# Performance work log

Measured on AMD Instinct MI355X. Metric: run time of the kernel, lower is better.

## Reference

```python
import jax, jax.numpy as jnp
import numpy as np

DIM = 2048
H = 16
QLR = 1536
KVLR = 512
NOPE = 128
ROPE = 64
VH = 128
QKH = NOPE + ROPE  # 192
B, S = 2, 2048
EPS = 1e-6


def _rmsnorm(x, w):
    return x * jax.lax.rsqrt(jnp.mean(x * x, axis=-1, keepdims=True) + EPS) * w


def _rope_cos_sin(seq_len, r, dtype):
    inv_freq = 1.0 / (10000.0 ** (jnp.arange(0, r, 2, dtype=jnp.float32) / r))
    ang = jnp.arange(seq_len, dtype=jnp.float32)[:, None] * inv_freq  # [S, r/2]
    return jnp.cos(ang).astype(dtype), jnp.sin(ang).astype(dtype)


def _rot(t, cos, sin):
    # rotate-half RoPE on last dim; cos/sin pre-broadcast to t's rank
    t1, t2 = jnp.split(t, 2, axis=-1)
    return jnp.concatenate([t1 * cos - t2 * sin, t2 * cos + t1 * sin], axis=-1)


def setup_inputs() -> dict:
    key = jax.random.key(0)
    ks = jax.random.split(key, 12)
    sd = 0.02
    return {
        "x": jax.random.normal(ks[0], (B, S, DIM), jnp.float32),
        "wqd": jax.random.normal(ks[1], (DIM, QLR), jnp.float32) * sd,
        "bqd": jnp.zeros((QLR,), jnp.float32),
        "qnorm_w": jnp.ones((QLR,), jnp.float32),
        "wqu": jax.random.normal(ks[2], (QLR, H * QKH), jnp.float32) * sd,
        "bqu": jnp.zeros((H * QKH,), jnp.float32),
        "wkvd": jax.random.normal(ks[3], (DIM, KVLR + ROPE), jnp.float32) * sd,
        "bkvd": jnp.zeros((KVLR + ROPE,), jnp.float32),
        "kvnorm_w": jnp.ones((KVLR,), jnp.float32),
        "wkvu": jax.random.normal(ks[4], (KVLR, H * (NOPE + VH)), jnp.float32) * sd,
        "bkvu": jnp.zeros((H * (NOPE + VH),), jnp.float32),
        "wout": jax.random.normal(ks[5], (H * VH, DIM), jnp.float32) * sd,
        "bout": jnp.zeros((DIM,), jnp.float32),
    }


def reference(x, wqd, bqd, qnorm_w, wqu, bqu, wkvd, bkvd, kvnorm_w, wkvu, bkvu, wout, bout):
    b, s, _ = x.shape
    # Q path: low-rank down, RMSNorm, up; split nope / rope
    q = _rmsnorm(x @ wqd + bqd, qnorm_w) @ wqu + bqu        # [b,s,H*QKH]
    q = q.reshape(b, s, H, QKH)
    q_nope, q_rope = q[..., :NOPE], q[..., NOPE:]
    # KV path: joint down-proj -> kv latent + shared rope key
    kvd = x @ wkvd + bkvd                                   # [b,s,KVLR+ROPE]
    kv_lora, k_rope = kvd[..., :KVLR], kvd[..., KVLR:]
    cos, sin = _rope_cos_sin(s, ROPE, x.dtype)
    q_rope = _rot(q_rope, cos[None, :, None, :], sin[None, :, None, :])
    k_rope = _rot(k_rope, cos[None, :, :], sin[None, :, :])  # [b,s,ROPE]
    kvu = _rmsnorm(kv_lora, kvnorm_w) @ wkvu + bkvu          # [b,s,H*(NOPE+VH)]
    kvu = kvu.reshape(b, s, H, NOPE + VH)
    k_nope, v = kvu[..., :NOPE], kvu[..., NOPE:]
    k_rope_b = jnp.broadcast_to(k_rope[:, :, None, :], (b, s, H, ROPE))
    qf = jnp.concatenate([q_nope, q_rope], axis=-1)          # [b,s,H,QKH]
    kf = jnp.concatenate([k_nope, k_rope_b], axis=-1)        # [b,s,H,QKH]
    scale = QKH ** -0.5
    scores = jnp.einsum('bqhd,bkhd->bhqk', qf, kf) * scale
    causal = jnp.tril(jnp.ones((s, s), bool))
    scores = jnp.where(causal, scores, jnp.finfo(scores.dtype).min)
    attn = jax.nn.softmax(scores, axis=-1)
    o = jnp.einsum('bhqk,bkhd->bqhd', attn, v).reshape(b, s, H * VH)
    return o @ wout + bout
```

## Files before the change

### kernel.cpp

```cpp
#include <hip/hip_runtime.h>
#include <hip/hip_bf16.h>
#include <math.h>

#define HH 16
#define SS 2048
#define BBATCH 2
#define NROWS 4096

typedef __attribute__((ext_vector_type(8))) __bf16 bf16x8;
typedef __attribute__((ext_vector_type(4))) float f32x4;
typedef const __attribute__((address_space(1))) unsigned int* gas1_t;
typedef __attribute__((address_space(3))) unsigned int* las3_t;

__device__ __forceinline__ unsigned short f2bf(float f) {
  unsigned u = __builtin_bit_cast(unsigned, f);
  u += 0x7fffu + ((u >> 16) & 1u);
  return (unsigned short)(u >> 16);
}

__device__ __forceinline__ void gload16(const void* g, void* l) {
  __builtin_amdgcn_global_load_lds((gas1_t)g, (las3_t)l, 16, 0, 0);
}
__device__ __forceinline__ f32x4 mfma16(bf16x8 a, bf16x8 b, f32x4 c) {
  return __builtin_amdgcn_mfma_f32_16x16x32_bf16(a, b, c, 0, 0, 0);
}

__global__ __launch_bounds__(256) void k_convert(const float* __restrict__ in,
                                                 unsigned short* __restrict__ out, long n4) {
  long i = (long)blockIdx.x * blockDim.x + threadIdx.x;
  long stride = (long)gridDim.x * blockDim.x;
  for (; i < n4; i += stride) {
    float4 v = ((const float4*)in)[i];
    ushort4 o = { f2bf(v.x), f2bf(v.y), f2bf(v.z), f2bf(v.w) };
    ((ushort4*)out)[i] = o;
  }
}

__global__ __launch_bounds__(256) void k_transpose(const float* __restrict__ W,
                                                   unsigned short* __restrict__ Wt,
                                                   int K, int N, int Npad) {
  __shared__ float tile[32][33];
  int n0 = blockIdx.x * 32, k0 = blockIdx.y * 32;
  int tx = threadIdx.x & 31, ty = threadIdx.x >> 5;
  for (int i = ty; i < 32; i += 8) {
    int k = k0 + i, n = n0 + tx;
    tile[i][tx] = (k < K && n < N) ? W[(long)k * N + n] : 0.f;
  }
  __syncthreads();
  for (int i = ty; i < 32; i += 8) {
    int n = n0 + i, k = k0 + tx;
    if (n < Npad && k < K) Wt[(long)n * K + k] = f2bf(tile[tx][i]);
  }
}

__global__ __launch_bounds__(256) void k_bias_merge(const float* __restrict__ bqd,
                                                    const float* __restrict__ bkvd,
                                                    float* __restrict__ mb) {
  int i = blockIdx.x * 256 + threadIdx.x;
  if (i < 2176) mb[i] = i < 1536 ? bqd[i] : (i < 2112 ? bkvd[i - 1536] : 0.f);
}

__global__ __launch_bounds__(64) void k_rope_table(float2* __restrict__ tab) {
  int s = blockIdx.x * 2 + (threadIdx.x >> 5);
  int i = threadIdx.x & 31;
  float inv = powf(10000.f, -(float)i / 32.f);
  float ang = (float)s * inv;
  float sn, cs;
  sincosf(ang, &sn, &cs);
  tab[s * 32 + i] = make_float2(cs, sn);
}

__global__ __launch_bounds__(256) void k_gemm(const unsigned short* __restrict__ A,
                                              const unsigned short* __restrict__ Bt,
                                              const float* __restrict__ bias,
                                              float* __restrict__ C,
                                              int M, int N, int K) {
  __shared__ unsigned short lA[128 * 32];
  __shared__ unsigned short lB[128 * 32];
  int tid = threadIdx.x;
  int wave = tid >> 6, lane = tid & 63;
  int l15 = lane & 15, lhi = lane >> 4;
  int ntn = (N + 127) >> 7;
  int tm = blockIdx.x / ntn, tn = blockIdx.x % ntn;
  long row0 = (long)tm * 128, col0 = (long)tn * 128;
  int wr = wave >> 1, wc = wave & 1;

  const unsigned short* gA = A + (row0 + (tid >> 2)) * K + (tid & 3) * 8;
  const unsigned short* gB = Bt + (col0 + (tid >> 2)) * K + (tid & 3) * 8;
  unsigned short* lA0 = &lA[tid * 8];
  unsigned short* lB0 = &lB[tid * 8];

  f32x4 acc[4][4] = {};
  for (int k0 = 0; k0 < K; k0 += 32) {
    __syncthreads();
    gload16(gA + k0, lA0);
    gload16(gA + (long)64 * K + k0, lA0 + 2048);
    gload16(gB + k0, lB0);
    gload16(gB + (long)64 * K + k0, lB0 + 2048);
    asm volatile("s_waitcnt vmcnt(0)" ::: "memory");
    __syncthreads();
    bf16x8 af[4], bfr[4];
#pragma unroll
    for (int i = 0; i < 4; ++i) {
      af[i]  = *(const bf16x8*)&lA[(wr * 64 + i * 16 + l15) * 32 + lhi * 8];
      bfr[i] = *(const bf16x8*)&lB[(wc * 64 + i * 16 + l15) * 32 + lhi * 8];
    }
#pragma unroll
    for (int i = 0; i < 4; ++i)
#pragma unroll
      for (int j = 0; j < 4; ++j)
        acc[i][j] = mfma16(af[i], bfr[j], acc[i][j]);
  }
#pragma unroll
  for (int i = 0; i < 4; ++i)
#pragma unroll
    for (int j = 0; j < 4; ++j) {
      long r = row0 + wr * 64 + i * 16 + lhi * 4;
      long c = col0 + wc * 64 + j * 16 + l15;
      if (c < N) {
        float bv = bias[c];
#pragma unroll
        for (int rr = 0; rr < 4; ++rr)
          C[(r + rr) * N + c] = acc[i][j][rr] + bv;
      }
    }
}

__global__ __launch_bounds__(256) void k_gemm_qf(const unsigned short* __restrict__ A,
                                                 const unsigned short* __restrict__ Bt,
                                                 const float* __restrict__ bias,
                                                 const float2* __restrict__ rtab,
                                                 unsigned short* __restrict__ qf,
                                                 int M, int N, int K) {
  __shared__ unsigned short lA[128 * 32];
  __shared__ unsigned short lB[128 * 32];
  int tid = threadIdx.x;
  int wave = tid >> 6, lane = tid & 63;
  int l15 = lane & 15, lhi = lane >> 4;
  int ntn = (N + 127) >> 7;
  int tm = blockIdx.x / ntn, tn = blockIdx.x % ntn;
  long row0 = (long)tm * 128, col0 = (long)tn * 128;
  int wr = wave >> 1, wc = wave & 1;

  const unsigned short* gA = A + (row0 + (tid >> 2)) * K + (tid & 3) * 8;
  const unsigned short* gB = Bt + (col0 + (tid >> 2)) * K + (tid & 3) * 8;
  unsigned short* lA0 = &lA[tid * 8];
  unsigned short* lB0 = &lB[tid * 8];

  f32x4 acc[4][4] = {};
  for (int k0 = 0; k0 < K; k0 += 32) {
    __syncthreads();
    gload16(gA + k0, lA0);
    gload16(gA + (long)64 * K + k0, lA0 + 2048);
    gload16(gB + k0, lB0);
    gload16(gB + (long)64 * K + k0, lB0 + 2048);
    asm volatile("s_waitcnt vmcnt(0)" ::: "memory");
    __syncthreads();
    bf16x8 af[4], bfr[4];
#pragma unroll
    for (int i = 0; i < 4; ++i) {
      af[i]  = *(const bf16x8*)&lA[(wr * 64 + i * 16 + l15) * 32 + lhi * 8];
      bfr[i] = *(const bf16x8*)&lB[(wc * 64 + i * 16 + l15) * 32 + lhi * 8];
    }
#pragma unroll
    for (int i = 0; i < 4; ++i)
#pragma unroll
      for (int j = 0; j < 4; ++j)
        acc[i][j] = mfma16(af[i], bfr[j], acc[i][j]);
  }

  const float scq = 0.07216878364870322f * 1.4426950408889634f;
  int base = (int)col0 + wc * 64;
  int h = base / 192;
  int m192 = base - h * 192;
  float bv[4];
#pragma unroll
  for (int j = 0; j < 4; ++j) bv[j] = bias[base + j * 16 + l15];

#pragma unroll
  for (int i = 0; i < 4; ++i) {
#pragma unroll
    for (int rr = 0; rr < 4; ++rr) {
      long r = row0 + wr * 64 + i * 16 + lhi * 4 + rr;
      int s = (int)(r & 2047), b = (int)(r >> 11);
      unsigned short* dst = qf + (((long)(b * HH + h)) * SS + s) * 192;
      if (m192 < 128) {
#pragma unroll
        for (int j = 0; j < 4; ++j)
          dst[m192 + j * 16 + l15] = f2bf((acc[i][j][rr] + bv[j]) * scq);
      } else {
#pragma unroll
        for (int j = 0; j < 2; ++j) {
          int ifq = j * 16 + l15;
          float2 cs = rtab[s * 32 + ifq];
          float v1 = acc[i][j][rr] + bv[j];
          float v2 = acc[i][j + 2][rr] + bv[j + 2];
          dst[128 + ifq] = f2bf((v1 * cs.x - v2 * cs.y) * scq);
          dst[160 + ifq] = f2bf((v2 * cs.x + v1 * cs.y) * scq);
        }
      }
    }
  }
}

__global__ __launch_bounds__(256) void k_gemm_kv(const unsigned short* __restrict__ A,
                                                 const unsigned short* __restrict__ Bt,
                                                 const float* __restrict__ bias,
                                                 unsigned short* __restrict__ kf3,
                                                 unsigned short* __restrict__ vt3,
                                                 int M, int N, int K) {
  __shared__ unsigned short smem[16384];
  unsigned short* lA = smem;
  unsigned short* lB = smem + 4096;
  int tid = threadIdx.x;
  int wave = tid >> 6, lane = tid & 63;
  int l15 = lane & 15, lhi = lane >> 4;
  int ntn = N >> 7;
  int tm = blockIdx.x / ntn, tn = blockIdx.x % ntn;
  long row0 = (long)tm * 128, col0 = (long)tn * 128;
  int wr = wave >> 1, wc = wave & 1;

  const unsigned short* gA = A + (row0 + (tid >> 2)) * K + (tid & 3) * 8;
  const unsigned short* gB = Bt + (col0 + (tid >> 2)) * K + (tid & 3) * 8;
  unsigned short* lA0 = &lA[tid * 8];
  unsigned short* lB0 = &lB[tid * 8];

  f32x4 acc[4][4] = {};
  for (int k0 = 0; k0 < K; k0 += 32) {
    __syncthreads();
    gload16(gA + k0, lA0);
    gload16(gA + (long)64 * K + k0, lA0 + 2048);
    gload16(gB + k0, lB0);
    gload16(gB + (long)64 * K + k0, lB0 + 2048);
    asm volatile("s_waitcnt vmcnt(0)" ::: "memory");
    __syncthreads();
    bf16x8 af[4], bfr[4];
#pragma unroll
    for (int i = 0; i < 4; ++i) {
      af[i]  = *(const bf16x8*)&lA[(wr * 64 + i * 16 + l15) * 32 + lhi * 8];
      bfr[i] = *(const bf16x8*)&lB[(wc * 64 + i * 16 + l15) * 32 + lhi * 8];
    }
#pragma unroll
    for (int i = 0; i < 4; ++i)
#pragma unroll
      for (int j = 0; j < 4; ++j)
        acc[i][j] = mfma16(af[i], bfr[j], acc[i][j]);
  }

  int base = (int)col0 + wc * 64;
  int h = base >> 8;
  bool isv = (base & 255) >= 128;
  float bv[4];
#pragma unroll
  for (int j = 0; j < 4; ++j) bv[j] = bias[base + j * 16 + l15];

  int b = (int)(row0 >> 11);
  long bh = (long)b * HH + h;
  int lrb = wr * 64;
  __syncthreads();

  if (isv) {
#pragma unroll
    for (int i = 0; i < 4; ++i) {
      int lr = lrb + i * 16 + lhi * 4;
#pragma unroll
      for (int j = 0; j < 4; ++j) {
        int lc = wc * 64 + j * 16 + l15;
        ushort4 pk = { f2bf(acc[i][j][0] + bv[j]), f2bf(acc[i][j][1] + bv[j]),
                       f2bf(acc[i][j][2] + bv[j]), f2bf(acc[i][j][3] + bv[j]) };
        *(ushort4*)&smem[((lr >> 5) << 12) + lc * 32 + (lr & 31)] = pk;
      }
    }
    __syncthreads();
    long dst0 = (bh * 64 + ((row0 & 2047) >> 5)) * 4096;
#pragma unroll
    for (int p = 0; p < 8; ++p) {
      int e = p * 256 + tid;
      *(uint4*)&vt3[dst0 + e * 8] = *(uint4*)&smem[e * 8];
    }
  } else {
#pragma unroll
    for (int i = 0; i < 4; ++i) {
      int lr0 = lrb + i * 16 + lhi * 4;
#pragma unroll
      for (int j = 0; j < 4; ++j) {
        int c = (base & 255) + j * 16 + l15;
        int tbase = ((lr0 >> 4) << 11) + ((c >> 5) << 9) + (((c >> 3) & 3) << 7) + (c & 7);
#pragma unroll
        for (int rr = 0; rr < 4; ++rr)
          smem[tbase + ((lr0 + rr) & 15) * 8] = f2bf(acc[i][j][rr] + bv[j]);
      }
    }
    __syncthreads();
    long kb3 = (bh * 128 + ((row0 & 2047) >> 4)) * 3072;
#pragma unroll
    for (int p = 0; p < 8; ++p) {
      int e = p * 256 + tid;
      int tile = e >> 6;
      int off = (e & 63) * 8;
      long dst = kb3 + ((long)(tile >> 2) * 6 + (tile & 3)) * 512 + off;
      *(uint4*)&kf3[dst] = *(uint4*)&smem[tile * 512 + off];
    }
  }
}

__global__ __launch_bounds__(256) void k_rmsnorm(const float* __restrict__ X,
                                                 const float* __restrict__ w,
                                                 unsigned short* __restrict__ Y,
                                                 int L, int ldx) {
  long row = blockIdx.x;
  const float* x = X + row * ldx;
  float ss = 0.f;
  int n4 = L >> 2;
  for (int i = threadIdx.x; i < n4; i += 256) {
    float4 v = ((const float4*)x)[i];
    ss += v.x * v.x + v.y * v.y + v.z * v.z + v.w * v.w;
  }
  for (int off = 32; off > 0; off >>= 1) ss += __shfl_xor(ss, off);
  __shared__ float sb[4];
  if ((threadIdx.x & 63) == 0) sb[threadIdx.x >> 6] = ss;
  __syncthreads();
  float scale = rsqrtf((sb[0] + sb[1] + sb[2] + sb[3]) / (float)L + 1e-6f);
  unsigned short* y = Y + row * L;
  for (int i = threadIdx.x; i < L; i += 256)
    y[i] = f2bf(x[i] * scale * w[i]);
}

__global__ __launch_bounds__(64) void k_extract_krope(const float* __restrict__ sC,
                                                      unsigned short* __restrict__ kf3) {
  int bs = blockIdx.x;
  int lane = threadIdx.x;
  int s = bs & (SS - 1), b = bs >> 11;
  const float* src = sC + (long)bs * 2176 + 2048;
  int i = lane & 31;
  float inv = powf(10000.f, -(float)i / 32.f);
  float ang = (float)s * inv;
  float sn, cs;
  sincosf(ang, &sn, &cs);
  float t1 = src[i], t2 = src[32 + i];
  float v = (lane < 32) ? (t1 * cs - t2 * sn) : (t2 * cs + t1 * sn);
  unsigned short bv = f2bf(v);
  int d = 128 + lane;
  long inner = (long)(d >> 5) * 512 + ((d >> 3) & 3) * 128 + (s & 15) * 8 + (d & 7);
#pragma unroll
  for (int h = 0; h < HH; ++h) {
    long blk = ((long)(b * HH + h) * 128 + (s >> 4)) * 6;
    kf3[blk * 512 + inner] = bv;
  }
}

__global__ __launch_bounds__(256, 4) void k_attn(const unsigned short* __restrict__ qf,
                                                 const unsigned short* __restrict__ kf3,
                                                 const unsigned short* __restrict__ vt3,
                                                 unsigned short* __restrict__ o) {
  __shared__ unsigned short kbuf[64 * 192];
  __shared__ unsigned short pbuf[4][16 * 72];
  int tid = threadIdx.x;
  int wave = tid >> 6, lane = tid & 63;
  int l15 = lane & 15, lhi = lane >> 4;
  int idx = blockIdx.x;
  int g = idx >> 8, j = idx & 255;
  int a = j >> 5, bh = j & 31;
  int qt = g < 2 ? (g == 0 ? a : a + 8) : (g == 2 ? 23 - a : 31 - a);
  int b = bh >> 4, h = bh & 15;
  int q0 = qt * 64;
  int nt = qt + 1;
  const char* kbase = (const char*)(kf3 + (long)bh * 128 * 3072);
  const unsigned short* vfrag0 = vt3 + (long)bh * 64 * 4096 + l15 * 32 + lhi * 8;
  const unsigned short* kread = kbuf + lane * 8;

  {
    const char* src = kbase + tid * 16;
    char* dst = (char*)kbuf + tid * 16;
#pragma unroll
    for (int p = 0; p < 6; ++p) gload16(src + p * 4096, dst + p * 4096);
  }

  const unsigned short* Qb = qf + ((long)bh * SS + q0 + wave * 16 + l15) * 192 + lhi * 8;
  bf16x8 qfr[6];
#pragma unroll
  for (int ks = 0; ks < 6; ++ks) qfr[ks] = *(const bf16x8*)(Qb + ks * 32);

  float m = -3e38f, ls = 0.f;
  f32x4 acc[8] = {};
  int qin = wave * 16 + l15;

  for (int t = 0; t < nt; ++t) {
    asm volatile("s_waitcnt vmcnt(0)" ::: "memory");
    __builtin_amdgcn_s_barrier();
    __builtin_amdgcn_sched_barrier(0);

    f32x4 sc[4] = {};
    __builtin_amdgcn_s_setprio(1);
#pragma unroll
    for (int ks = 0; ks < 6; ++ks) {
      bf16x8 kfr[4];
#pragma unroll
      for (int nf = 0; nf < 4; ++nf)
        kfr[nf] = *(const bf16x8*)&kread[(nf * 6 + ks) * 512];
#pragma unroll
      for (int nf = 0; nf < 4; ++nf)
        sc[nf] = mfma16(kfr[nf], qfr[ks], sc[nf]);
    }
    __builtin_amdgcn_s_setprio(0);
    __builtin_amdgcn_sched_barrier(0);
    __builtin_amdgcn_s_barrier();
    __builtin_amdgcn_sched_barrier(0);

    const unsigned short* vtb = vfrag0 + (long)t * 8192;
    bf16x8 v0[8];
#pragma unroll
    for (int nf = 0; nf < 8; ++nf) v0[nf] = *(const bf16x8*)(vtb + nf * 512);
    __builtin_amdgcn_sched_barrier(0);

    if (t + 1 < nt) {
      const char* src = kbase + (long)(t + 1) * 24576 + tid * 16;
      char* dst = (char*)kbuf + tid * 16;
#pragma unroll
      for (int p = 0; p < 6; ++p) gload16(src + p * 4096, dst + p * 4096);
    }

    bool diag = (t == nt - 1);
    float mnf[4];
#pragma unroll
    for (int nf = 0; nf < 4; ++nf) {
      if (diag) {
#pragma unroll
        for (int jj = 0; jj < 4; ++jj) {
          int kin = nf * 16 + lhi * 4 + jj;
          if (kin > qin) sc[nf][jj] = -3e38f;
        }
      }
      mnf[nf] = fmaxf(fmaxf(sc[nf][0], sc[nf][1]), fmaxf(sc[nf][2], sc[nf][3]));
    }
    float mx = fmaxf(fmaxf(mnf[0], mnf[1]), fmaxf(mnf[2], mnf[3]));
    mx = fmaxf(mx, __shfl_xor(mx, 16));
    mx = fmaxf(mx, __shfl_xor(mx, 32));
    if (!__all(mx <= m + 8.f)) {
      float mn = fmaxf(m, mx);
      float alpha = exp2f(m - mn);
      m = mn;
      ls *= alpha;
#pragma unroll
      for (int nf = 0; nf < 8; ++nf)
#pragma unroll
        for (int jj = 0; jj < 4; ++jj) acc[nf][jj] *= alpha;
    }
    float pnf[4];
#pragma unroll
    for (int nf = 0; nf < 4; ++nf) {
      float e0 = exp2f(sc[nf][0] - m), e1 = exp2f(sc[nf][1] - m);
      float e2 = exp2f(sc[nf][2] - m), e3 = exp2f(sc[nf][3] - m);
      pnf[nf] = (e0 + e1) + (e2 + e3);
      ushort4 pk = { f2bf(e0), f2bf(e1), f2bf(e2), f2bf(e3) };
      *(ushort4*)&pbuf[wave][l15 * 72 + nf * 16 + lhi * 4] = pk;
    }
    float ps = (pnf[0] + pnf[1]) + (pnf[2] + pnf[3]);
    ps += __shfl_xor(ps, 16);
    ps += __shfl_xor(ps, 32);
    ls += ps;

    {
      bf16x8 pf = *(const bf16x8*)&pbuf[wave][l15 * 72 + lhi * 8];
      __builtin_amdgcn_s_setprio(1);
#pragma unroll
      for (int nf = 0; nf < 8; ++nf) acc[nf] = mfma16(v0[nf], pf, acc[nf]);
      __builtin_amdgcn_s_setprio(0);
    }
    bf16x8 v1[8];
#pragma unroll
    for (int nf = 0; nf < 8; ++nf) v1[nf] = *(const bf16x8*)(vtb + 4096 + nf * 512);
    {
      bf16x8 pf = *(const bf16x8*)&pbuf[wave][l15 * 72 + 32 + lhi * 8];
      __builtin_amdgcn_s_setprio(1);
#pragma unroll
      for (int nf = 0; nf < 8; ++nf) acc[nf] = mfma16(v1[nf], pf, acc[nf]);
      __builtin_amdgcn_s_setprio(0);
    }
  }

  float invl = 1.f / ls;
  long orow = (long)b * SS + q0 + wave * 16 + l15;
#pragma unroll
  for (int nf = 0; nf < 8; ++nf) {
    ushort4 ov = { f2bf(acc[nf][0] * invl), f2bf(acc[nf][1] * invl),
                   f2bf(acc[nf][2] * invl), f2bf(acc[nf][3] * invl) };
    *(ushort4*)&o[orow * 2048 + h * 128 + nf * 16 + lhi * 4] = ov;
  }
}

extern "C" void kernel_launch(void* const* d_in, const int* in_sizes, int n_in,
                              void* d_out, int out_size, void* d_ws, size_t ws_size,
                              hipStream_t stream) {
  const float* x    = (const float*)d_in[0];
  const float* wqd  = (const float*)d_in[1];
  const float* bqd  = (const float*)d_in[2];
  const float* qnw  = (const float*)d_in[3];
  const float* wqu  = (const float*)d_in[4];
  const float* bqu  = (const float*)d_in[5];
  const float* wkvd = (const float*)d_in[6];
  const float* bkvd = (const float*)d_in[7];
  const float* kvnw = (const float*)d_in[8];
  const float* wkvu = (const float*)d_in[9];
  const float* bkvu = (const float*)d_in[10];
  const float* wout = (const float*)d_in[11];
  const float* bout = (const float*)d_in[12];
  float* out = (float*)d_out;

  char* ws = (char*)d_ws;
  size_t off = 0;
  auto alloc = [&](size_t sz) {
    char* p = ws + off;
    off += (sz + 255) & ~(size_t)255;
    return p;
  };
  unsigned short* xb    = (unsigned short*)alloc((size_t)NROWS * 2048 * 2);
  unsigned short* wqkt  = (unsigned short*)alloc((size_t)2176 * 2048 * 2);
  unsigned short* wqut  = (unsigned short*)alloc((size_t)3072 * 1536 * 2);
  unsigned short* wkvut = (unsigned short*)alloc((size_t)4096 * 512 * 2);
  unsigned short* woutt = (unsigned short*)alloc((size_t)2048 * 2048 * 2);
  unsigned short* qn    = (unsigned short*)alloc((size_t)NROWS * 1536 * 2);
  unsigned short* kvn   = (unsigned short*)alloc((size_t)NROWS * 512 * 2);
  unsigned short* qfb   = (unsigned short*)alloc((size_t)32 * SS * 192 * 2);
  unsigned short* kfb   = (unsigned short*)alloc((size_t)32 * SS * 192 * 2);
  unsigned short* vtb   = (unsigned short*)alloc((size_t)32 * 128 * SS * 2);
  unsigned short* ob    = (unsigned short*)alloc((size_t)NROWS * 2048 * 2);
  float*  mbias = (float*)alloc((size_t)2176 * 4);
  float2* rtab  = (float2*)alloc((size_t)SS * 32 * 8);
  float* sC = (float*)alloc((size_t)NROWS * 2176 * 4);

  k_convert<<<2048, 256, 0, stream>>>(x, xb, (long)NROWS * 2048 / 4);
  k_transpose<<<dim3(48, 64), 256, 0, stream>>>(wqd, wqkt, 2048, 1536, 1536);
  k_transpose<<<dim3(20, 64), 256, 0, stream>>>(wkvd, wqkt + (size_t)1536 * 2048, 2048, 576, 640);
  k_transpose<<<dim3(96, 48), 256, 0, stream>>>(wqu, wqut, 1536, 3072, 3072);
  k_transpose<<<dim3(128, 16), 256, 0, stream>>>(wkvu, wkvut, 512, 4096, 4096);
  k_transpose<<<dim3(64, 64), 256, 0, stream>>>(wout, woutt, 2048, 2048, 2048);
  k_bias_merge<<<9, 256, 0, stream>>>(bqd, bkvd, mbias);
  k_rope_table<<<SS / 2, 64, 0, stream>>>(rtab);

  k_gemm<<<32 * 17, 256, 0, stream>>>(xb, wqkt, mbias, sC, NROWS, 2176, 2048);

  k_rmsnorm<<<NROWS, 256, 0, stream>>>(sC, qnw, qn, 1536, 2176);
  k_gemm_qf<<<32 * 24, 256, 0, stream>>>(qn, wqut, bqu, rtab, qfb, NROWS, 3072, 1536);

  k_rmsnorm<<<NROWS, 256, 0, stream>>>(sC + 1536, kvnw, kvn, 512, 2176);
  k_extract_krope<<<NROWS, 64, 0, stream>>>(sC, kfb);
  k_gemm_kv<<<32 * 32, 256, 0, stream>>>(kvn, wkvut, bkvu, kfb, vtb, NROWS, 4096, 512);

  k_attn<<<1024, 256, 0, stream>>>(qfb, kfb, vtb, ob);

  k_gemm<<<32 * 16, 256, 0, stream>>>(ob, woutt, bout, out, NROWS, 2048, 2048);
}
```

Before: 424.3 us.

## Split long causal attention rows into two KV halves with a merge kernel

Query tiles 8-31 now have their KV range split into two halves, each processed by a separate block. Each block writes unnormalized fp32 partial outputs plus running max and sum to workspace. A new merge kernel combines the two halves with softmax rescaling. Short tiles 0-7 are still done whole. This evens out per-block work and raises the block count from 1024 to 1792 to cut the tail imbalance of causal attention. The cost is extra fp32 partial traffic and one more kernel launch.

```diff
diff --git a/kernel.cpp b/kernel.cpp
--- a/kernel.cpp
+++ b/kernel.cpp
@@ -352,25 +352,41 @@
 __global__ __launch_bounds__(256, 4) void k_attn(const unsigned short* __restrict__ qf,
                                                  const unsigned short* __restrict__ kf3,
                                                  const unsigned short* __restrict__ vt3,
-                                                 unsigned short* __restrict__ o) {
+                                                 unsigned short* __restrict__ o,
+                                                 float* __restrict__ pO,
+                                                 float* __restrict__ pml) {
   __shared__ unsigned short kbuf[64 * 192];
   __shared__ unsigned short pbuf[4][16 * 72];
   int tid = threadIdx.x;
   int wave = tid >> 6, lane = tid & 63;
   int l15 = lane & 15, lhi = lane >> 4;
   int idx = blockIdx.x;
-  int g = idx >> 8, j = idx & 255;
-  int a = j >> 5, bh = j & 31;
-  int qt = g < 2 ? (g == 0 ? a : a + 8) : (g == 2 ? 23 - a : 31 - a);
+  int rp = idx >> 5, bh = idx & 31;
+  int qt, t0, t1, item;
+  bool dodiag;
+  if (rp < 48) {
+    qt = 31 - (rp >> 1);
+    int part = rp & 1;
+    int h0 = (qt + 1) >> 1;
+    t0 = part ? h0 : 0;
+    t1 = part ? qt + 1 : h0;
+    item = (bh * 24 + (qt - 8)) * 2 + part;
+    dodiag = (part == 1);
+  } else {
+    qt = 55 - rp;
+    t0 = 0;
+    t1 = qt + 1;
+    item = -1;
+    dodiag = true;
+  }
   int b = bh >> 4, h = bh & 15;
   int q0 = qt * 64;
-  int nt = qt + 1;
   const char* kbase = (const char*)(kf3 + (long)bh * 128 * 3072);
   const unsigned short* vfrag0 = vt3 + (long)bh * 64 * 4096 + l15 * 32 + lhi * 8;
   const unsigned short* kread = kbuf + lane * 8;
 
   {
-    const char* src = kbase + tid * 16;
+    const char* src = kbase + (long)t0 * 24576 + tid * 16;
     char* dst = (char*)kbuf + tid * 16;
 #pragma unroll
     for (int p = 0; p < 6; ++p) gload16(src + p * 4096, dst + p * 4096);
@@ -385,7 +401,7 @@
   f32x4 acc[8] = {};
   int qin = wave * 16 + l15;
 
-  for (int t = 0; t < nt; ++t) {
+  for (int t = t0; t < t1; ++t) {
     asm volatile("s_waitcnt vmcnt(0)" ::: "memory");
     __builtin_amdgcn_s_barrier();
     __builtin_amdgcn_sched_barrier(0);
@@ -413,14 +429,14 @@
     for (int nf = 0; nf < 8; ++nf) v0[nf] = *(const bf16x8*)(vtb + nf * 512);
     __builtin_amdgcn_sched_barrier(0);
 
-    if (t + 1 < nt) {
+    if (t + 1 < t1) {
       const char* src = kbase + (long)(t + 1) * 24576 + tid * 16;
       char* dst = (char*)kbuf + tid * 16;
 #pragma unroll
       for (int p = 0; p < 6; ++p) gload16(src + p * 4096, dst + p * 4096);
     }
 
-    bool diag = (t == nt - 1);
+    bool diag = dodiag && (t == t1 - 1);
     float mnf[4];
 #pragma unroll
     for (int nf = 0; nf < 4; ++nf) {
@@ -479,13 +495,60 @@
     }
   }
 
-  float invl = 1.f / ls;
-  long orow = (long)b * SS + q0 + wave * 16 + l15;
-#pragma unroll
-  for (int nf = 0; nf < 8; ++nf) {
-    ushort4 ov = { f2bf(acc[nf][0] * invl), f2bf(acc[nf][1] * invl),
-                   f2bf(acc[nf][2] * invl), f2bf(acc[nf][3] * invl) };
-    *(ushort4*)&o[orow * 2048 + h * 128 + nf * 16 + lhi * 4] = ov;
+  int qloc = wave * 16 + l15;
+  if (item < 0) {
+    float invl = 1.f / ls;
+    long orow = (long)b * SS + q0 + qloc;
+#pragma unroll
+    for (int nf = 0; nf < 8; ++nf) {
+      ushort4 ov = { f2bf(acc[nf][0] * invl), f2bf(acc[nf][1] * invl),
+                     f2bf(acc[nf][2] * invl), f2bf(acc[nf][3] * invl) };
+      *(ushort4*)&o[orow * 2048 + h * 128 + nf * 16 + lhi * 4] = ov;
+    }
+  } else {
+    float* po = pO + (long)item * 8192 + qloc * 128;
+#pragma unroll
+    for (int nf = 0; nf < 8; ++nf)
+      *(float4*)&po[nf * 16 + lhi * 4] = __builtin_bit_cast(float4, acc[nf]);
+    if (lhi == 0) {
+      pml[(long)item * 128 + qloc * 2] = m;
+      pml[(long)item * 128 + qloc * 2 + 1] = ls;
+    }
+  }
+}
+
+__global__ __launch_bounds__(256) void k_merge(const float* __restrict__ pO,
+                                               const float* __restrict__ pml,
+                                               unsigned short* __restrict__ o) {
+  int item2 = blockIdx.x;
+  int bh = item2 / 24, qt = (item2 % 24) + 8;
+  int b = bh >> 4, h = bh & 15;
+  int q0 = qt * 64;
+  long i0 = (long)item2 * 2, i1 = i0 + 1;
+  __shared__ float w0s[64], w1s[64];
+  int tid = threadIdx.x;
+  if (tid < 64) {
+    float m0 = pml[i0 * 128 + tid * 2], ls0 = pml[i0 * 128 + tid * 2 + 1];
+    float m1 = pml[i1 * 128 + tid * 2], ls1 = pml[i1 * 128 + tid * 2 + 1];
+    float mm = fmaxf(m0, m1);
+    float w0 = exp2f(m0 - mm), w1 = exp2f(m1 - mm);
+    float inv = 1.f / (ls0 * w0 + ls1 * w1);
+    w0s[tid] = w0 * inv;
+    w1s[tid] = w1 * inv;
+  }
+  __syncthreads();
+  const float* p0 = pO + i0 * 8192;
+  const float* p1 = pO + i1 * 8192;
+#pragma unroll
+  for (int p = 0; p < 8; ++p) {
+    int e = p * 256 + tid;
+    int q = e >> 5, d4 = (e & 31) * 4;
+    float4 a = *(const float4*)&p0[q * 128 + d4];
+    float4 c = *(const float4*)&p1[q * 128 + d4];
+    float w0 = w0s[q], w1 = w1s[q];
+    ushort4 ov = { f2bf(a.x * w0 + c.x * w1), f2bf(a.y * w0 + c.y * w1),
+                   f2bf(a.z * w0 + c.z * w1), f2bf(a.w * w0 + c.w * w1) };
+    *(ushort4*)&o[((long)b * SS + q0 + q) * 2048 + h * 128 + d4] = ov;
   }
 }
 
@@ -527,6 +590,8 @@
   unsigned short* ob    = (unsigned short*)alloc((size_t)NROWS * 2048 * 2);
   float*  mbias = (float*)alloc((size_t)2176 * 4);
   float2* rtab  = (float2*)alloc((size_t)SS * 32 * 8);
+  float*  pO    = (float*)alloc((size_t)32 * 24 * 2 * 8192 * 4);
+  float*  pml   = (float*)alloc((size_t)32 * 24 * 2 * 128 * 4);
   float* sC = (float*)alloc((size_t)NROWS * 2176 * 4);
 
   k_convert<<<2048, 256, 0, stream>>>(x, xb, (long)NROWS * 2048 / 4);
@@ -547,7 +612,8 @@
   k_extract_krope<<<NROWS, 64, 0, stream>>>(sC, kfb);
   k_gemm_kv<<<32 * 32, 256, 0, stream>>>(kvn, wkvut, bkvu, kfb, vtb, NROWS, 4096, 512);
 
-  k_attn<<<1024, 256, 0, stream>>>(qfb, kfb, vtb, ob);
+  k_attn<<<1792, 256, 0, stream>>>(qfb, kfb, vtb, ob, pO, pml);
+  k_merge<<<768, 256, 0, stream>>>(pO, pml, ob);
 
   k_gemm<<<32 * 16, 256, 0, stream>>>(ob, woutt, bout, out, NROWS, 2048, 2048);
 }
```

After: 415.0 us. 2.2% less time.
